# Kernel tuning notes

Measured on AMD Instinct MI355X. Metric: run time of the kernel, lower is better.

The kernel has to match this reference:

```python
import jax, jax.numpy as jnp
import numpy as np

B, L, H, W, C = 2, 16, 64, 64, 256


def _pconv(x5, Wm, b):
    # 1x1x1 Conv3d == pointwise channel linear. x5: (B,C,L,H,W), Wm: (Cout,Cin), b: (Cout,)
    return jnp.einsum('bclhw,oc->bolhw', x5, Wm) + b[None, :, None, None, None]


def setup_inputs() -> dict:
    key = jax.random.key(0)
    ks = jax.random.split(key, 9)
    s = 0.02  # small init so softmax logits (sum over HW=4096) stay in a sane range
    x = jax.random.normal(ks[0], (B, L, H, W, C), jnp.float32)
    prev_features = jax.random.normal(ks[1], (B, L, H, W, C), jnp.float32)
    Wq = jax.random.normal(ks[2], (C, C), jnp.float32) * s
    bq = jax.random.normal(ks[3], (C,), jnp.float32) * s
    Wk = jax.random.normal(ks[4], (C, C), jnp.float32) * s
    bk = jax.random.normal(ks[5], (C,), jnp.float32) * s
    Wv = jax.random.normal(ks[6], (C, C), jnp.float32) * s
    bv = jax.random.normal(ks[7], (C,), jnp.float32) * s
    gamma = jnp.array([0.5], jnp.float32)  # torch init is 0; use 0.5 so the attention path is exercised
    return {'x': x, 'prev_features': prev_features, 'Wq': Wq, 'bq': bq,
            'Wk': Wk, 'bk': bk, 'Wv': Wv, 'bv': bv, 'gamma': gamma}


def reference(x, prev_features, Wq, bq, Wk, bk, Wv, bv, gamma):
    # x, prev_features: (B, L, H, W, C) channel-last
    x5 = jnp.transpose(x, (0, 4, 1, 2, 3))              # (B,C,L,H,W)
    p5 = jnp.transpose(prev_features, (0, 4, 1, 2, 3))  # (B,C,L,H,W)
    b_, c_, l_, h_, w_ = x5.shape
    n = b_ * l_
    hw = h_ * w_
    # Q: (B,C,L,H,W)->(B,L,C,H,W)->(BL, C, HW)
    q = jnp.transpose(_pconv(x5, Wq, bq), (0, 2, 1, 3, 4)).reshape(n, c_, hw)
    # K: (B,C,L,H,W)->(B,L,C,W,H)->(BL, C, HW)  (note W,H swap before flatten, as in torch)
    k = jnp.transpose(_pconv(p5, Wk, bk), (0, 2, 1, 4, 3)).reshape(n, c_, hw)
    # attention[n,c,d] = sum_s q[n,c,s] * k[n,d,s]  -> (BL, C, C), softmax over d
    attn = jax.nn.softmax(jnp.einsum('ncs,nds->ncd', q, k), axis=-1)
    # V: raw contiguous reshape of (B,C,L,H,W) into (BL, C, HW) -- faithful to torch's buggy reshape
    v = _pconv(p5, Wv, bv).reshape(n, c_, hw)
    # out[n,s,c] = sum_d v[n,d,s] * attn[n,c,d]   (== bmm(v^T, attn^T))
    out = jnp.einsum('nds,ncd->nsc', v, attn).reshape(b_, l_, h_, w_, c_)
    # x5.permute(0,2,3,4,1) recovers the original x
    return gamma * out + x
```

## Files before the change

### kernel.cpp

```cpp
#include <hip/hip_runtime.h>
#include <hip/hip_bf16.h>


typedef short short8 __attribute__((ext_vector_type(8)));
typedef short short4v __attribute__((ext_vector_type(4)));
typedef float f32x4 __attribute__((ext_vector_type(4)));

static __device__ __forceinline__ unsigned short f2bf(float f) {
  union { __hip_bfloat16 h; unsigned short u; } cv;
  cv.h = __float2bfloat16(f);
  return cv.u;
}

__global__ __launch_bounds__(256) void k_convert_w(const float* __restrict__ wq,
                                                   const float* __restrict__ wk,
                                                   const float* __restrict__ wv,
                                                   unsigned short* __restrict__ o) {
  int i = blockIdx.x * 256 + threadIdx.x;
  const float* s = (i < 65536) ? wq : (i < 131072 ? wk : wv);
  o[i] = f2bf(s[i & 65535]);
}

template <int MODE>
__global__ __launch_bounds__(256) void k_qkv(const float* __restrict__ src,
                                             const unsigned short* __restrict__ w,
                                             const float* __restrict__ bias,
                                             unsigned short* __restrict__ dst) {
  __shared__ __align__(16) unsigned short inp[64 * 264];
  __shared__ __align__(16) unsigned short wc[256 * 72];
  const int t = threadIdx.x;
  int n, wcol, s0;
  if (MODE == 1) {
    n = blockIdx.x >> 6; wcol = blockIdx.x & 63; s0 = 0;
  } else {
    n = blockIdx.x >> 6; wcol = 0; s0 = (blockIdx.x & 63) << 6;
  }
#pragma unroll
  for (int i = 0; i < 16; ++i) {
    int q = i * 256 + t;
    int row = q >> 6;
    int c4 = (q & 63) << 2;
    size_t srow = (MODE == 1) ? (size_t)(n * 4096 + row * 64 + wcol)
                              : (size_t)(n * 4096 + s0 + row);
    float4 v = *(const float4*)(src + srow * 256 + c4);
    unsigned short* p = &inp[row * 264 + c4];
    p[0] = f2bf(v.x); p[1] = f2bf(v.y); p[2] = f2bf(v.z); p[3] = f2bf(v.w);
  }
  const int wid = t >> 6, lane = t & 63;
  const int l16 = lane & 15, lk = (lane >> 4) << 3;
  f32x4 acc[16];
#pragma unroll
  for (int i = 0; i < 16; ++i) acc[i] = (f32x4){0.f, 0.f, 0.f, 0.f};
  const unsigned short* arow = &inp[(wid * 16 + l16) * 264];
  const int wo = t >> 3, wch = t & 7;
  for (int kc = 0; kc < 4; ++kc) {
    __syncthreads();
#pragma unroll
    for (int p = 0; p < 8; ++p) {
      const int o = p * 32 + wo;
      short8 wv = *(const short8*)(w + o * 256 + kc * 64 + wch * 8);
      *(short8*)&wc[o * 72 + wch * 8] = wv;
    }
    __syncthreads();
#pragma unroll
    for (int ks2 = 0; ks2 < 64; ks2 += 32) {
      short8 a = *(const short8*)(arow + kc * 64 + ks2 + lk);
#pragma unroll
      for (int nt = 0; nt < 16; ++nt) {
        short8 b = *(const short8*)(&wc[(nt * 16 + l16) * 72 + ks2 + lk]);
        acc[nt] = __builtin_amdgcn_mfma_f32_16x16x32_bf16(a, b, acc[nt], 0, 0, 0);
      }
    }
  }
  __syncthreads();
  const int sl0 = wid * 16 + ((lane >> 4) << 2);
#pragma unroll
  for (int nt = 0; nt < 16; ++nt) {
    const int o = nt * 16 + l16;
    const float bo = bias[o];
    short4v pk;
#pragma unroll
    for (int j = 0; j < 4; ++j) pk[j] = (short)f2bf(acc[nt][j] + bo);
    *(short4v*)&wc[o * 72 + sl0] = pk;
  }
  __syncthreads();
  const int co = t >> 3, ch = t & 7;
#pragma unroll
  for (int p = 0; p < 8; ++p) {
    const int o = p * 32 + co;
    short8 v = *(const short8*)&wc[o * 72 + ch * 8];
    size_t base;
    if (MODE == 0) {
      base = ((size_t)n << 20) + (size_t)o * 4096 + (size_t)(s0 + ch * 8);
    } else if (MODE == 1) {
      base = ((size_t)n << 20) + (size_t)o * 4096 + (size_t)(wcol * 64 + ch * 8);
    } else {
      const int b_ = n >> 4, l_ = n & 15;
      base = (size_t)((b_ * 256 + o) * 16 + l_) * 4096 + (size_t)(s0 + ch * 8);
    }
    *(short8*)(dst + base) = v;
  }
}

__global__ __launch_bounds__(256) void k_vt(const unsigned short* __restrict__ vb,
                                            unsigned short* __restrict__ vt) {
  __shared__ unsigned short lds[64 * 264];
  const int t = threadIdx.x;
  const int np = blockIdx.x >> 6;
  const int s0 = (blockIdx.x & 63) << 6;
  const int b = np >> 4, chi = np & 15;
  const int d0 = (t & 127) << 1, sh = (t >> 7) << 5;
  const int c = chi * 16 + (d0 >> 4);
  const int l0 = d0 & 15;
  const unsigned short* r0p = vb + (size_t)((b * 256 + c) * 16 + l0) * 4096 + s0 + sh;
  const unsigned short* r1p = r0p + 4096;
#pragma unroll
  for (int i = 0; i < 4; ++i) {
    short8 a = *(const short8*)(r0p + i * 8);
    short8 bb = *(const short8*)(r1p + i * 8);
#pragma unroll
    for (int j = 0; j < 8; ++j) {
      int s = sh + i * 8 + j;
      unsigned int pk = (unsigned int)(unsigned short)a[j] |
                        ((unsigned int)(unsigned short)bb[j] << 16);
      *(unsigned int*)&lds[s * 264 + d0] = pk;
    }
  }
  __syncthreads();
  const int sl = t >> 2, ch = t & 3;
  unsigned short* outp = vt + ((size_t)np << 20) + (size_t)(s0 + sl) * 256 + ch * 64;
  const unsigned short* lp = &lds[sl * 264 + ch * 64];
#pragma unroll
  for (int i = 0; i < 8; ++i)
    *(short8*)(outp + i * 8) = *(const short8*)(lp + i * 8);
}

__global__ __launch_bounds__(256) void k_logits(const unsigned short* __restrict__ qb,
                                                const unsigned short* __restrict__ kb,
                                                float* __restrict__ attn) {
  const int n = blockIdx.z;
  const int c0 = blockIdx.x * 64, d0 = blockIdx.y * 64;
  const int t = threadIdx.x, wid = t >> 6, lane = t & 63;
  const int l16 = lane & 15, lk = (lane >> 4) << 3;
  const unsigned short* qrow = qb + (size_t)n * 1048576 + (size_t)(c0 + wid * 16 + l16) * 4096 + lk;
  const unsigned short* krow = kb + (size_t)n * 1048576 + (size_t)(d0 + l16) * 4096 + lk;
  f32x4 acc[4];
#pragma unroll
  for (int i = 0; i < 4; ++i) acc[i] = (f32x4){0.f, 0.f, 0.f, 0.f};
#pragma unroll 4
  for (int ks = 0; ks < 4096; ks += 32) {
    short8 a = *(const short8*)(qrow + ks);
#pragma unroll
    for (int nt = 0; nt < 4; ++nt) {
      short8 b = *(const short8*)(krow + nt * 16 * 4096 + ks);
      acc[nt] = __builtin_amdgcn_mfma_f32_16x16x32_bf16(a, b, acc[nt], 0, 0, 0);
    }
  }
  const int crow = c0 + wid * 16 + ((lane >> 4) << 2);
#pragma unroll
  for (int nt = 0; nt < 4; ++nt)
#pragma unroll
    for (int j = 0; j < 4; ++j)
      attn[(size_t)n * 65536 + (size_t)(crow + j) * 256 + (size_t)(d0 + nt * 16 + l16)] = acc[nt][j];
}

__global__ __launch_bounds__(256) void k_softmax(const float* __restrict__ attn,
                                                 unsigned short* __restrict__ abf) {
  const int t = threadIdx.x, wid = t >> 6, lane = t & 63;
  const int row = blockIdx.x * 4 + wid;
  const int n = row >> 8, c = row & 255;
  const float* p = attn + (size_t)n * 65536 + (size_t)c * 256;
  float v0 = p[lane], v1 = p[lane + 64], v2 = p[lane + 128], v3 = p[lane + 192];
  float m = fmaxf(fmaxf(v0, v1), fmaxf(v2, v3));
#pragma unroll
  for (int off = 32; off >= 1; off >>= 1) m = fmaxf(m, __shfl_xor(m, off, 64));
  float e0 = __expf(v0 - m), e1 = __expf(v1 - m), e2 = __expf(v2 - m), e3 = __expf(v3 - m);
  float s = e0 + e1 + e2 + e3;
#pragma unroll
  for (int off = 32; off >= 1; off >>= 1) s += __shfl_xor(s, off, 64);
  const float inv = 1.0f / s;
  unsigned short* q = abf + (size_t)n * 65536 + (size_t)c * 256;
  q[lane]       = f2bf(e0 * inv);
  q[lane + 64]  = f2bf(e1 * inv);
  q[lane + 128] = f2bf(e2 * inv);
  q[lane + 192] = f2bf(e3 * inv);
}

__global__ __launch_bounds__(256) void k_out(const unsigned short* __restrict__ vT,
                                             const unsigned short* __restrict__ abf,
                                             const float* __restrict__ x,
                                             const float* __restrict__ gamma,
                                             float* __restrict__ out) {
  __shared__ __align__(16) unsigned short bsm[64 * 264];
  const int n = blockIdx.z;
  const int c0 = blockIdx.y * 64;
  const int s0 = blockIdx.x * 64;
  const int t = threadIdx.x, wid = t >> 6, lane = t & 63;
  const int l16 = lane & 15, lk = (lane >> 4) << 3;
  {
    const int rr = t >> 5, ch = t & 31;
#pragma unroll
    for (int i = 0; i < 8; ++i) {
      const int row = rr + i * 8;
      short8 v = *(const short8*)(abf + (size_t)n * 65536 + (size_t)(c0 + row) * 256 + ch * 8);
      *(short8*)&bsm[row * 264 + ch * 8] = v;
    }
  }
  __syncthreads();
  const unsigned short* arow = vT + (size_t)n * 1048576 + (size_t)(s0 + wid * 16 + l16) * 256 + lk;
  f32x4 acc[4];
#pragma unroll
  for (int i = 0; i < 4; ++i) acc[i] = (f32x4){0.f, 0.f, 0.f, 0.f};
#pragma unroll
  for (int ks = 0; ks < 256; ks += 32) {
    short8 a = *(const short8*)(arow + ks);
#pragma unroll
    for (int nt = 0; nt < 4; ++nt) {
      short8 b = *(const short8*)(&bsm[(nt * 16 + l16) * 264 + ks + lk]);
      acc[nt] = __builtin_amdgcn_mfma_f32_16x16x32_bf16(a, b, acc[nt], 0, 0, 0);
    }
  }
  __syncthreads();
  float* ldsf = (float*)bsm;
  const int sl0 = wid * 16 + ((lane >> 4) << 2);
#pragma unroll
  for (int nt = 0; nt < 4; ++nt)
#pragma unroll
    for (int j = 0; j < 4; ++j)
      ldsf[(sl0 + j) * 68 + nt * 16 + l16] = acc[nt][j];
  __syncthreads();
  const float g = gamma[0];
  const int ch = t & 15, rr = t >> 4;
#pragma unroll
  for (int i = 0; i < 4; ++i) {
    const int row = rr + i * 16;
    f32x4 v = *(const f32x4*)&ldsf[row * 68 + ch * 4];
    const size_t addr = ((size_t)n * 4096 + (size_t)(s0 + row)) * 256 + (size_t)(c0 + ch * 4);
    float4 xv = *(const float4*)(x + addr);
    float4 ov;
    ov.x = g * v[0] + xv.x; ov.y = g * v[1] + xv.y;
    ov.z = g * v[2] + xv.z; ov.w = g * v[3] + xv.w;
    *(float4*)(out + addr) = ov;
  }
}

extern "C" void kernel_launch(void* const* d_in, const int* in_sizes, int n_in,
                              void* d_out, int out_size, void* d_ws, size_t ws_size,
                              hipStream_t stream) {
  const float* x    = (const float*)d_in[0];
  const float* prev = (const float*)d_in[1];
  const float* Wq   = (const float*)d_in[2];
  const float* bq   = (const float*)d_in[3];
  const float* Wk   = (const float*)d_in[4];
  const float* bk   = (const float*)d_in[5];
  const float* Wv   = (const float*)d_in[6];
  const float* bv   = (const float*)d_in[7];
  const float* gamma = (const float*)d_in[8];

  char* ws = (char*)d_ws;
  unsigned short* qv   = (unsigned short*)ws;
  unsigned short* kbuf = (unsigned short*)(ws + 67108864ULL);
  float* attn          = (float*)(ws + 134217728ULL);
  unsigned short* abf  = (unsigned short*)(ws + 142606336ULL);
  unsigned short* wbf  = (unsigned short*)(ws + 146800640ULL);

  k_convert_w<<<dim3(768), dim3(256), 0, stream>>>(Wq, Wk, Wv, wbf);
  k_qkv<0><<<dim3(2048), dim3(256), 0, stream>>>(x, wbf, bq, qv);
  k_qkv<1><<<dim3(2048), dim3(256), 0, stream>>>(prev, wbf + 65536, bk, kbuf);
  k_logits<<<dim3(4, 4, 32), dim3(256), 0, stream>>>(qv, kbuf, attn);
  k_qkv<2><<<dim3(2048), dim3(256), 0, stream>>>(prev, wbf + 131072, bv, kbuf);
  k_softmax<<<dim3(2048), dim3(256), 0, stream>>>(attn, abf);
  k_vt<<<dim3(2048), dim3(256), 0, stream>>>(kbuf, qv);
  k_out<<<dim3(64, 4, 32), dim3(256), 0, stream>>>(qv, abf, x, gamma, (float*)d_out);
}
```

Before: 656.9 us.

## Tile logits GEMM through double-buffered LDS with split-K and swizzle

Rewrites the Q·K^T logits kernel so that 64x128 tiles are staged into LDS with global_load_lds. The LDS buffers are double-buffered and XOR-swizzled, and each wave computes a 32x64 sub-tile instead of reading operands directly from global memory. The K dimension is split in two across blockIdx.y, which writes two partial logit buffers. The softmax kernel now sums those partials. This targets redundant global reads and low data reuse in the old direct-load loop, at the cost of an extra 8 MB partial buffer plus extra softmax reads, and it shifts the workspace offsets.

```diff
diff --git a/kernel.cpp b/kernel.cpp
--- a/kernel.cpp
+++ b/kernel.cpp
@@ -138,30 +138,96 @@
 __global__ __launch_bounds__(256) void k_logits(const unsigned short* __restrict__ qb,
                                                 const unsigned short* __restrict__ kb,
                                                 float* __restrict__ attn) {
+  __shared__ __align__(16) unsigned short qt[2][64 * 64];
+  __shared__ __align__(16) unsigned short kt[2][128 * 64];
   const int n = blockIdx.z;
-  const int c0 = blockIdx.x * 64, d0 = blockIdx.y * 64;
+  const int kh = blockIdx.y;
+  const int c0 = (blockIdx.x >> 1) * 64;
+  const int d0 = (blockIdx.x & 1) * 128;
   const int t = threadIdx.x, wid = t >> 6, lane = t & 63;
-  const int l16 = lane & 15, lk = (lane >> 4) << 3;
-  const unsigned short* qrow = qb + (size_t)n * 1048576 + (size_t)(c0 + wid * 16 + l16) * 4096 + lk;
-  const unsigned short* krow = kb + (size_t)n * 1048576 + (size_t)(d0 + l16) * 4096 + lk;
-  f32x4 acc[4];
-#pragma unroll
-  for (int i = 0; i < 4; ++i) acc[i] = (f32x4){0.f, 0.f, 0.f, 0.f};
-#pragma unroll 4
-  for (int ks = 0; ks < 4096; ks += 32) {
-    short8 a = *(const short8*)(qrow + ks);
+  const int l16 = lane & 15, l4 = lane >> 4;
+  const int wr = wid >> 1, wc = wid & 1;
+  const int koff0 = kh * 2048;
+  const unsigned short* qg = qb + ((size_t)n << 20) + (size_t)c0 * 4096 + koff0;
+  const unsigned short* kg = kb + ((size_t)n << 20) + (size_t)d0 * 4096 + koff0;
+  const int srow8 = wid * 8 + (lane >> 3);
+  const int schunk = lane & 7;
+
+  int arow[2], brow[4];
+#pragma unroll
+  for (int mt = 0; mt < 2; ++mt) arow[mt] = wr * 32 + mt * 16 + l16;
+#pragma unroll
+  for (int nt = 0; nt < 4; ++nt) brow[nt] = wc * 64 + nt * 16 + l16;
+
+  f32x4 acc[2][4];
+#pragma unroll
+  for (int mt = 0; mt < 2; ++mt)
+#pragma unroll
+    for (int nt = 0; nt < 4; ++nt) acc[mt][nt] = (f32x4){0.f, 0.f, 0.f, 0.f};
+
+#define STAGE(buf, kc)                                                          \
+  {                                                                             \
+    const int ko = (kc) * 64;                                                   \
+    _Pragma("unroll")                                                           \
+    for (int i = 0; i < 2; ++i) {                                               \
+      const int row = i * 32 + srow8;                                           \
+      const int cg = schunk ^ (row & 7);                                        \
+      const unsigned short* g = qg + (size_t)row * 4096 + ko + cg * 8;          \
+      unsigned short* l = &qt[buf][i * 2048 + wid * 512];                       \
+      __builtin_amdgcn_global_load_lds(                                         \
+          (const __attribute__((address_space(1))) unsigned int*)(const void*)g,\
+          (__attribute__((address_space(3))) unsigned int*)(void*)l, 16, 0, 0); \
+    }                                                                           \
+    _Pragma("unroll")                                                           \
+    for (int i = 0; i < 4; ++i) {                                               \
+      const int row = i * 32 + srow8;                                           \
+      const int cg = schunk ^ (row & 7);                                        \
+      const unsigned short* g = kg + (size_t)row * 4096 + ko + cg * 8;          \
+      unsigned short* l = &kt[buf][i * 2048 + wid * 512];                       \
+      __builtin_amdgcn_global_load_lds(                                         \
+          (const __attribute__((address_space(1))) unsigned int*)(const void*)g,\
+          (__attribute__((address_space(3))) unsigned int*)(void*)l, 16, 0, 0); \
+    }                                                                           \
+  }
+
+  int cur = 0;
+  STAGE(0, 0);
+  __syncthreads();
+  for (int kc = 0; kc < 32; ++kc) {
+    if (kc < 31) STAGE(cur ^ 1, kc + 1);
+    short8 bf[4][2];
+#pragma unroll
+    for (int nt = 0; nt < 4; ++nt)
+#pragma unroll
+      for (int ks = 0; ks < 2; ++ks)
+        bf[nt][ks] = *(const short8*)&kt[cur][brow[nt] * 64 +
+                                             (((ks * 4 + l4) ^ (brow[nt] & 7)) << 3)];
+#pragma unroll
+    for (int mt = 0; mt < 2; ++mt) {
+      short8 a0 = *(const short8*)&qt[cur][arow[mt] * 64 + ((l4 ^ (arow[mt] & 7)) << 3)];
+      short8 a1 = *(const short8*)&qt[cur][arow[mt] * 64 + (((4 + l4) ^ (arow[mt] & 7)) << 3)];
+#pragma unroll
+      for (int nt = 0; nt < 4; ++nt) {
+        acc[mt][nt] = __builtin_amdgcn_mfma_f32_16x16x32_bf16(a0, bf[nt][0], acc[mt][nt], 0, 0, 0);
+        acc[mt][nt] = __builtin_amdgcn_mfma_f32_16x16x32_bf16(a1, bf[nt][1], acc[mt][nt], 0, 0, 0);
+      }
+    }
+    __syncthreads();
+    cur ^= 1;
+  }
+#undef STAGE
+  float* ah = attn + (size_t)kh * 2097152 + (size_t)n * 65536;
+#pragma unroll
+  for (int mt = 0; mt < 2; ++mt)
 #pragma unroll
     for (int nt = 0; nt < 4; ++nt) {
-      short8 b = *(const short8*)(krow + nt * 16 * 4096 + ks);
-      acc[nt] = __builtin_amdgcn_mfma_f32_16x16x32_bf16(a, b, acc[nt], 0, 0, 0);
-    }
-  }
-  const int crow = c0 + wid * 16 + ((lane >> 4) << 2);
-#pragma unroll
-  for (int nt = 0; nt < 4; ++nt)
-#pragma unroll
-    for (int j = 0; j < 4; ++j)
-      attn[(size_t)n * 65536 + (size_t)(crow + j) * 256 + (size_t)(d0 + nt * 16 + l16)] = acc[nt][j];
+      const int d = d0 + wc * 64 + nt * 16 + l16;
+#pragma unroll
+      for (int j = 0; j < 4; ++j) {
+        const int c = c0 + wr * 32 + mt * 16 + (l4 << 2) + j;
+        ah[(size_t)c * 256 + d] = acc[mt][nt][j];
+      }
+    }
 }
 
 __global__ __launch_bounds__(256) void k_softmax(const float* __restrict__ attn,
@@ -169,8 +235,12 @@
   const int t = threadIdx.x, wid = t >> 6, lane = t & 63;
   const int row = blockIdx.x * 4 + wid;
   const int n = row >> 8, c = row & 255;
-  const float* p = attn + (size_t)n * 65536 + (size_t)c * 256;
-  float v0 = p[lane], v1 = p[lane + 64], v2 = p[lane + 128], v3 = p[lane + 192];
+  const float* p0 = attn + (size_t)n * 65536 + (size_t)c * 256;
+  const float* p1 = p0 + 2097152;
+  float v0 = p0[lane] + p1[lane];
+  float v1 = p0[lane + 64] + p1[lane + 64];
+  float v2 = p0[lane + 128] + p1[lane + 128];
+  float v3 = p0[lane + 192] + p1[lane + 192];
   float m = fmaxf(fmaxf(v0, v1), fmaxf(v2, v3));
 #pragma unroll
   for (int off = 32; off >= 1; off >>= 1) m = fmaxf(m, __shfl_xor(m, off, 64));
@@ -261,13 +331,13 @@
   unsigned short* qv   = (unsigned short*)ws;
   unsigned short* kbuf = (unsigned short*)(ws + 67108864ULL);
   float* attn          = (float*)(ws + 134217728ULL);
-  unsigned short* abf  = (unsigned short*)(ws + 142606336ULL);
-  unsigned short* wbf  = (unsigned short*)(ws + 146800640ULL);
+  unsigned short* abf  = (unsigned short*)(ws + 150994944ULL);
+  unsigned short* wbf  = (unsigned short*)(ws + 155189248ULL);
 
   k_convert_w<<<dim3(768), dim3(256), 0, stream>>>(Wq, Wk, Wv, wbf);
   k_qkv<0><<<dim3(2048), dim3(256), 0, stream>>>(x, wbf, bq, qv);
   k_qkv<1><<<dim3(2048), dim3(256), 0, stream>>>(prev, wbf + 65536, bk, kbuf);
-  k_logits<<<dim3(4, 4, 32), dim3(256), 0, stream>>>(qv, kbuf, attn);
+  k_logits<<<dim3(8, 2, 32), dim3(256), 0, stream>>>(qv, kbuf, attn);
   k_qkv<2><<<dim3(2048), dim3(256), 0, stream>>>(prev, wbf + 131072, bv, kbuf);
   k_softmax<<<dim3(2048), dim3(256), 0, stream>>>(attn, abf);
   k_vt<<<dim3(2048), dim3(256), 0, stream>>>(kbuf, qv);
```

Result: faster. 574.3 us (-12.6%).
